# Optimization experiments

Measured on AMD Instinct MI355X. Metric: run time of the kernel, lower is better.

The kernel has to match this reference:

```python
import jax, jax.numpy as jnp
import numpy as np

HIDDEN = 768
META = 25
ED_COUNT = 300
B, N_MENT, N_PAIRS = 2, 2000, 40000


def setup_inputs() -> dict:
    key = jax.random.key(0)
    ks = jax.random.split(key, 8)
    mention_reprs = jax.random.normal(ks[0], (B, N_MENT, HIDDEN), dtype=jnp.float32)
    coref_mention_pairs = jax.random.randint(ks[1], (B, N_PAIRS, 2), 0, N_MENT)
    coref_eds = jax.random.randint(ks[2], (B, N_PAIRS), 0, ED_COUNT)
    in_dim = HIDDEN * 2 + META
    # nn.Linear default init scale ~ 1/sqrt(fan_in); exact init is irrelevant for correctness
    W1 = jax.random.normal(ks[3], (in_dim, HIDDEN), dtype=jnp.float32) / np.sqrt(in_dim)
    b1 = jnp.zeros((HIDDEN,), dtype=jnp.float32)
    W2 = jax.random.normal(ks[4], (HIDDEN, 1), dtype=jnp.float32) / np.sqrt(HIDDEN)
    b2 = jnp.zeros((1,), dtype=jnp.float32)
    ed_table = jax.random.normal(ks[5], (ED_COUNT, META), dtype=jnp.float32)
    return {
        "mention_reprs": mention_reprs,
        "coref_mention_pairs": coref_mention_pairs,
        "coref_eds": coref_eds,
        "ed_table": ed_table,
        "W1": W1,
        "b1": b1,
        "W2": W2,
        "b2": b2,
    }


def reference(mention_reprs, coref_mention_pairs, coref_eds, ed_table, W1, b1, W2, b2):
    b = mention_reprs.shape[0]
    # batch_index gather: [B, P, 2, H]
    bidx = jnp.arange(b)[:, None, None]
    pairs = mention_reprs[bidx, coref_mention_pairs]
    # flatten pair dim -> [B, P, 2H]
    pair_repr = pairs.reshape(b, pairs.shape[1], -1)
    eds = ed_table[coref_eds]  # [B, P, META]
    coref_repr = jnp.concatenate([pair_repr, eds], axis=2)  # [B, P, 2H+META]
    h = jax.nn.relu(coref_repr @ W1 + b1)  # dropout = identity in eval
    logits = (h @ W2 + b2).squeeze(-1)  # [B, P]
    return logits
```

## Files before the change

kernel.cpp:

```cpp
#include <hip/hip_runtime.h>
#include <stdint.h>

#define HIDDEN 768
#define META 25
#define EDC 300
#define BB 2
#define NMENT 2000
#define NPAIRS 40000
#define M_ROWS (BB * NMENT)
#define M_PAD 4096
#define N_OUT 1536
#define TOTAL_PAIRS (BB * NPAIRS)
#define BK 64

typedef __bf16 bf16x8 __attribute__((ext_vector_type(8)));
typedef float f32x4 __attribute__((ext_vector_type(4)));

static __device__ __forceinline__ float bf2f(unsigned short u) {
    union { unsigned int u; float f; } v; v.u = ((unsigned int)u) << 16; return v.f;
}
static __device__ __forceinline__ float2 bf2x(unsigned int u) {
    union { unsigned int x; float f; } lo, hi;
    lo.x = u << 16; hi.x = u & 0xffff0000u;
    float2 r; r.x = lo.f; r.y = hi.f; return r;
}
static __device__ __forceinline__ unsigned short f2bf(float f) {
    union { float f; unsigned int u; } v; v.f = f;
    unsigned int u = v.u;
    unsigned int r = (u + 0x7FFFu + ((u >> 16) & 1u)) >> 16;
    return (unsigned short)r;
}

#define GLOAD_LDS16(g, l)                                                            \
    __builtin_amdgcn_global_load_lds((const __attribute__((address_space(1))) void*)(g), \
                                     (__attribute__((address_space(3))) void*)(l), 16, 0, 0)

#define NB_CONVM 3072
#define NB_CONVW 576
#define NB_PREP  900
#define NB_W2    3

__global__ __launch_bounds__(256) void k_prep_all(
        const float* __restrict__ M, unsigned short* __restrict__ Mb,
        const float* __restrict__ W1, unsigned short* __restrict__ Wt,
        const float* __restrict__ ed_table, const float* __restrict__ b1,
        unsigned short* __restrict__ Epp,
        const float* __restrict__ W2, unsigned short* __restrict__ W2b) {
    const int blk = blockIdx.x;
    const int t = threadIdx.x;
    if (blk < NB_CONVM) {
        int idx = (blk * 256 + t) * 4;
        int row = idx / HIDDEN;
        ushort4 o;
        if (row < M_ROWS) {
            const float4 v = *(const float4*)(M + idx);
            o.x = f2bf(v.x); o.y = f2bf(v.y); o.z = f2bf(v.z); o.w = f2bf(v.w);
        } else {
            o.x = 0; o.y = 0; o.z = 0; o.w = 0;
        }
        *(ushort4*)(Mb + idx) = o;
    } else if (blk < NB_CONVM + NB_CONVW) {
        __shared__ float tile[32][68];
        int id = blk - NB_CONVM;
        int nt = id % 24, kt = id / 24;
        int n0 = nt * 64, k0 = kt * 32;
        int tk = t >> 4, tn = (t & 15) * 4;
        int srcRowOff = (n0 < HIDDEN) ? 0 : HIDDEN;
        int srcColBase = (n0 < HIDDEN) ? n0 : (n0 - HIDDEN);
        {
            const float4 v0 = *(const float4*)(W1 + (size_t)(k0 + tk + srcRowOff) * HIDDEN + srcColBase + tn);
            tile[tk][tn] = v0.x; tile[tk][tn + 1] = v0.y; tile[tk][tn + 2] = v0.z; tile[tk][tn + 3] = v0.w;
            const float4 v1 = *(const float4*)(W1 + (size_t)(k0 + tk + 16 + srcRowOff) * HIDDEN + srcColBase + tn);
            tile[tk + 16][tn] = v1.x; tile[tk + 16][tn + 1] = v1.y; tile[tk + 16][tn + 2] = v1.z; tile[tk + 16][tn + 3] = v1.w;
        }
        __syncthreads();
        int wn = t >> 2, wk = (t & 3) * 8;
        unsigned int p0 = (unsigned int)f2bf(tile[wk + 0][wn]) | ((unsigned int)f2bf(tile[wk + 1][wn]) << 16);
        unsigned int p1 = (unsigned int)f2bf(tile[wk + 2][wn]) | ((unsigned int)f2bf(tile[wk + 3][wn]) << 16);
        unsigned int p2 = (unsigned int)f2bf(tile[wk + 4][wn]) | ((unsigned int)f2bf(tile[wk + 5][wn]) << 16);
        unsigned int p3 = (unsigned int)f2bf(tile[wk + 6][wn]) | ((unsigned int)f2bf(tile[wk + 7][wn]) << 16);
        uint4 pk; pk.x = p0; pk.y = p1; pk.z = p2; pk.w = p3;
        *(uint4*)(Wt + (size_t)(n0 + wn) * HIDDEN + k0 + wk) = pk;
    } else if (blk < NB_CONVM + NB_CONVW + NB_PREP) {
        int id = (blk - NB_CONVM - NB_CONVW) * 256 + t;
        int e = id / HIDDEN, n = id - e * HIDDEN;
        float acc = b1[n];
#pragma unroll
        for (int k = 0; k < META; k++)
            acc += ed_table[e * META + k] * W1[(size_t)(2 * HIDDEN + k) * HIDDEN + n];
        Epp[id] = f2bf(acc);
    } else {
        int id = (blk - NB_CONVM - NB_CONVW - NB_PREP) * 256 + t;
        if (id < HIDDEN) W2b[id] = f2bf(W2[id]);
    }
}

__global__ __launch_bounds__(256) void k_gemm(const unsigned short* __restrict__ Mb,
                                              const unsigned short* __restrict__ Wt,
                                              unsigned short* __restrict__ AW) {
    __shared__ unsigned short As[128 * BK];
    __shared__ unsigned short Bs[64 * BK];
    const int m0 = blockIdx.x * 128;
    const int n0 = blockIdx.y * 64;
    const int t = threadIdx.x, w = t >> 6, lane = t & 63;
    const int wm = (w & 1) * 64, wn = (w >> 1) * 32;
    const int q = lane >> 4, r = lane & 15;
    const int lrow = lane >> 3;
    const int lcol = ((((lane & 7) - lrow) & 7)) * 8;
    const unsigned short* gA = Mb + (size_t)(m0 + w * 32 + lrow) * HIDDEN + lcol;
    const unsigned short* gB = Wt + (size_t)(n0 + w * 16 + lrow) * HIDDEN + lcol;
    unsigned short* lA = As + (w * 32) * BK;
    unsigned short* lB = Bs + (w * 16) * BK;
    f32x4 acc[4][2] = {};
    for (int k0 = 0; k0 < HIDDEN; k0 += BK) {
        GLOAD_LDS16(gA + k0, lA);
        GLOAD_LDS16(gA + k0 + 8 * HIDDEN,  lA + 8 * BK);
        GLOAD_LDS16(gA + k0 + 16 * HIDDEN, lA + 16 * BK);
        GLOAD_LDS16(gA + k0 + 24 * HIDDEN, lA + 24 * BK);
        GLOAD_LDS16(gB + k0, lB);
        GLOAD_LDS16(gB + k0 + 8 * HIDDEN,  lB + 8 * BK);
        __syncthreads();
        bf16x8 af[4][2], bfr[2][2];
        const int rs = r & 7;
#pragma unroll
        for (int i = 0; i < 4; i++)
#pragma unroll
            for (int s = 0; s < 2; s++)
                af[i][s] = *(const bf16x8*)&As[(wm + i * 16 + r) * BK + 8 * ((q + 4 * s + rs) & 7)];
#pragma unroll
        for (int j = 0; j < 2; j++)
#pragma unroll
            for (int s = 0; s < 2; s++)
                bfr[j][s] = *(const bf16x8*)&Bs[(wn + j * 16 + r) * BK + 8 * ((q + 4 * s + rs) & 7)];
#pragma unroll
        for (int i = 0; i < 4; i++)
#pragma unroll
            for (int j = 0; j < 2; j++) {
                acc[i][j] = __builtin_amdgcn_mfma_f32_16x16x32_bf16(af[i][0], bfr[j][0], acc[i][j], 0, 0, 0);
                acc[i][j] = __builtin_amdgcn_mfma_f32_16x16x32_bf16(af[i][1], bfr[j][1], acc[i][j], 0, 0, 0);
            }
        __syncthreads();
    }
    const int colb = n0 + wn + (lane & 15);
    const int rowb = m0 + wm + (lane >> 4) * 4;
#pragma unroll
    for (int i = 0; i < 4; i++)
#pragma unroll
        for (int j = 0; j < 2; j++) {
            unsigned short* dst = AW + (size_t)(rowb + i * 16) * N_OUT + colb + j * 16;
#pragma unroll
            for (int reg = 0; reg < 4; reg++)
                dst[(size_t)reg * N_OUT] = f2bf(acc[i][j][reg]);
        }
}

__global__ __launch_bounds__(256, 6) void k_pair(const unsigned short* __restrict__ AW,
                                                 const unsigned short* __restrict__ Epp,
                                                 const unsigned short* __restrict__ W2b,
                                                 const float* __restrict__ b2,
                                                 const int* __restrict__ pairs,
                                                 const int* __restrict__ eds,
                                                 float* __restrict__ out) {
    const int wid = blockIdx.x * 4 + (threadIdx.x >> 6);
    const int lane = threadIdx.x & 63;
    const int hl = lane & 31;
    const bool lo = lane < 32;
    const int p0 = wid * 2;
    const size_t base = (p0 >= NPAIRS) ? (size_t)NMENT : 0;

    const int4 pr = *(const int4*)(pairs + (size_t)p0 * 2);
    const int2 e2 = *(const int2*)(eds + p0);

    const int n0 = lane * 8;
    const int n1 = 512 + hl * 8;

    const unsigned short* A1a = AW + (base + pr.x) * N_OUT;
    const unsigned short* A2a = AW + (base + pr.y) * N_OUT + HIDDEN;
    const unsigned short* EPa = Epp + (size_t)e2.x * HIDDEN;
    const unsigned short* A1b = AW + (base + pr.z) * N_OUT;
    const unsigned short* A2b = AW + (base + pr.w) * N_OUT + HIDDEN;
    const unsigned short* EPb = Epp + (size_t)e2.y * HIDDEN;

    const unsigned short* t1 = lo ? A1a : A1b;
    const unsigned short* t2 = lo ? A2a : A2b;
    const unsigned short* te = lo ? EPa : EPb;

    uint4 w0 = *(const uint4*)(W2b + n0);
    uint4 wc = *(const uint4*)(W2b + n1);
    uint4 x1 = *(const uint4*)(A1a + n0), x2 = *(const uint4*)(A2a + n0), xe = *(const uint4*)(EPa + n0);
    uint4 y1 = *(const uint4*)(A1b + n0), y2 = *(const uint4*)(A2b + n0), ye = *(const uint4*)(EPb + n0);
    uint4 q1 = *(const uint4*)(t1 + n1),  q2 = *(const uint4*)(t2 + n1),  qe = *(const uint4*)(te + n1);

    float accA = 0.f, accB = 0.f, tacc = 0.f;
#define ACC2(acc, ua, ub, ue, uw)                                              \
    {                                                                          \
        float2 fa = bf2x(ua), fb = bf2x(ub), fe = bf2x(ue), fw = bf2x(uw);     \
        float h0 = fmaxf(fa.x + fb.x + fe.x, 0.f);                             \
        float h1 = fmaxf(fa.y + fb.y + fe.y, 0.f);                             \
        acc += h0 * fw.x + h1 * fw.y;                                          \
    }
    ACC2(accA, x1.x, x2.x, xe.x, w0.x); ACC2(accA, x1.y, x2.y, xe.y, w0.y);
    ACC2(accA, x1.z, x2.z, xe.z, w0.z); ACC2(accA, x1.w, x2.w, xe.w, w0.w);
    ACC2(accB, y1.x, y2.x, ye.x, w0.x); ACC2(accB, y1.y, y2.y, ye.y, w0.y);
    ACC2(accB, y1.z, y2.z, ye.z, w0.z); ACC2(accB, y1.w, y2.w, ye.w, w0.w);
    ACC2(tacc, q1.x, q2.x, qe.x, wc.x); ACC2(tacc, q1.y, q2.y, qe.y, wc.y);
    ACC2(tacc, q1.z, q2.z, qe.z, wc.z); ACC2(tacc, q1.w, q2.w, qe.w, wc.w);
#undef ACC2

#pragma unroll
    for (int o = 32; o > 0; o >>= 1) {
        accA += __shfl_xor(accA, o, 64);
        accB += __shfl_xor(accB, o, 64);
    }
#pragma unroll
    for (int o = 16; o > 0; o >>= 1)
        tacc += __shfl_xor(tacc, o, 64);
    const float tA = __shfl(tacc, 0, 64);
    const float tB = __shfl(tacc, 32, 64);

    if (lane == 0) {
        float bias = b2[0];
        float2 o;
        o.x = accA + tA + bias;
        o.y = accB + tB + bias;
        *(float2*)(out + p0) = o;
    }
}

extern "C" void kernel_launch(void* const* d_in, const int* in_sizes, int n_in,
                              void* d_out, int out_size, void* d_ws, size_t ws_size,
                              hipStream_t stream) {
    const float* mention  = (const float*)d_in[0];
    const int*   pairs    = (const int*)d_in[1];
    const int*   eds      = (const int*)d_in[2];
    const float* ed_table = (const float*)d_in[3];
    const float* W1       = (const float*)d_in[4];
    const float* b1       = (const float*)d_in[5];
    const float* W2       = (const float*)d_in[6];
    const float* b2       = (const float*)d_in[7];
    float* out = (float*)d_out;

    char* ws = (char*)d_ws;
    unsigned short* Mb  = (unsigned short*)(ws);
    unsigned short* Wt  = (unsigned short*)(ws + 6291456);
    unsigned short* AW  = (unsigned short*)(ws + 8650752);
    unsigned short* Epp = (unsigned short*)(ws + 21233664);
    unsigned short* W2b = (unsigned short*)(ws + 21694464);

    k_prep_all<<<dim3(NB_CONVM + NB_CONVW + NB_PREP + NB_W2), dim3(256), 0, stream>>>(
        mention, Mb, W1, Wt, ed_table, b1, Epp, W2, W2b);
    k_gemm<<<dim3(M_PAD / 128, N_OUT / 64), dim3(256), 0, stream>>>(Mb, Wt, AW);
    k_pair<<<dim3(TOTAL_PAIRS / 8), dim3(256), 0, stream>>>(AW, Epp, W2b, b2, pairs, eds, out);
}
```

Baseline: 117.6 us.

## Bucket-sort mention pairs by row locality and swizzle pair blocks across XCDs

Adds a histogram pass (inside the prep kernel) and a scatter kernel that bucket the pairs by coarse first- and second-mention row indices, producing a permutation. The pair kernel walks pairs in that order, so the random row gathers from the projected mention table land on nearby rows. A block-index swizzle hands each XCD a contiguous range of buckets, aiming to raise L2 hit rates on those gathers. The cost is two extra kernel launches, global atomics, and an indirection load per pair, and outputs are now written as scattered scalar stores.

```diff
diff --git a/kernel.cpp b/kernel.cpp
--- a/kernel.cpp
+++ b/kernel.cpp
@@ -12,6 +12,7 @@
 #define N_OUT 1536
 #define TOTAL_PAIRS (BB * NPAIRS)
 #define BK 64
+#define NBUCKET 1024
 
 typedef __bf16 bf16x8 __attribute__((ext_vector_type(8)));
 typedef float f32x4 __attribute__((ext_vector_type(4)));
@@ -31,6 +32,10 @@
     return (unsigned short)r;
 }
 
+static __device__ __forceinline__ int pair_key(int2 pr, int p) {
+    return ((p >= NPAIRS) ? 512 : 0) | ((pr.x >> 6) << 4) | (pr.y >> 7);
+}
+
 #define GLOAD_LDS16(g, l)                                                            \
     __builtin_amdgcn_global_load_lds((const __attribute__((address_space(1))) void*)(g), \
                                      (__attribute__((address_space(3))) void*)(l), 16, 0, 0)
@@ -39,13 +44,20 @@
 #define NB_CONVW 576
 #define NB_PREP  900
 #define NB_W2    3
+#define NB_HIST  40
+
+__global__ __launch_bounds__(256) void k_zero(int* __restrict__ z) {
+#pragma unroll
+    for (int i = 0; i < 8; i++) z[i * 256 + threadIdx.x] = 0;
+}
 
 __global__ __launch_bounds__(256) void k_prep_all(
         const float* __restrict__ M, unsigned short* __restrict__ Mb,
         const float* __restrict__ W1, unsigned short* __restrict__ Wt,
         const float* __restrict__ ed_table, const float* __restrict__ b1,
         unsigned short* __restrict__ Epp,
-        const float* __restrict__ W2, unsigned short* __restrict__ W2b) {
+        const float* __restrict__ W2, unsigned short* __restrict__ W2b,
+        const int* __restrict__ pairs, int* __restrict__ hist) {
     const int blk = blockIdx.x;
     const int t = threadIdx.x;
     if (blk < NB_CONVM) {
@@ -89,9 +101,61 @@
         for (int k = 0; k < META; k++)
             acc += ed_table[e * META + k] * W1[(size_t)(2 * HIDDEN + k) * HIDDEN + n];
         Epp[id] = f2bf(acc);
-    } else {
+    } else if (blk < NB_CONVM + NB_CONVW + NB_PREP + NB_W2) {
         int id = (blk - NB_CONVM - NB_CONVW - NB_PREP) * 256 + t;
         if (id < HIDDEN) W2b[id] = f2bf(W2[id]);
+    } else {
+        __shared__ int lh[NBUCKET];
+        const int hb = blk - (NB_CONVM + NB_CONVW + NB_PREP + NB_W2);
+#pragma unroll
+        for (int i = 0; i < 4; i++) lh[i * 256 + t] = 0;
+        __syncthreads();
+#pragma unroll
+        for (int i = 0; i < 8; i++) {
+            int p = hb * 2048 + i * 256 + t;
+            if (p < TOTAL_PAIRS) {
+                int2 pr = *(const int2*)(pairs + (size_t)p * 2);
+                atomicAdd(&lh[pair_key(pr, p)], 1);
+            }
+        }
+        __syncthreads();
+#pragma unroll
+        for (int i = 0; i < 4; i++) {
+            int v = lh[i * 256 + t];
+            if (v) atomicAdd(&hist[i * 256 + t], v);
+        }
+    }
+}
+
+__global__ __launch_bounds__(256) void k_scatter(const int* __restrict__ pairs,
+                                                 const int* __restrict__ hist,
+                                                 int* __restrict__ cursor,
+                                                 int* __restrict__ perm) {
+    __shared__ int off[NBUCKET];
+    __shared__ int bsum[256];
+    const int t = threadIdx.x;
+    const int4 h = *(const int4*)(hist + t * 4);
+    const int s = h.x + h.y + h.z + h.w;
+    bsum[t] = s;
+    __syncthreads();
+    for (int o = 1; o < 256; o <<= 1) {
+        int v = (t >= o) ? bsum[t - o] : 0;
+        __syncthreads();
+        bsum[t] += v;
+        __syncthreads();
+    }
+    const int excl = bsum[t] - s;
+    off[t * 4 + 0] = excl;
+    off[t * 4 + 1] = excl + h.x;
+    off[t * 4 + 2] = excl + h.x + h.y;
+    off[t * 4 + 3] = excl + h.x + h.y + h.z;
+    __syncthreads();
+    const int p = blockIdx.x * 256 + t;
+    if (p < TOTAL_PAIRS) {
+        const int2 pr = *(const int2*)(pairs + (size_t)p * 2);
+        const int key = pair_key(pr, p);
+        const int rank = atomicAdd(&cursor[key], 1);
+        perm[off[key] + rank] = p;
     }
 }
 
@@ -160,26 +224,33 @@
                                                  const float* __restrict__ b2,
                                                  const int* __restrict__ pairs,
                                                  const int* __restrict__ eds,
+                                                 const int* __restrict__ perm,
                                                  float* __restrict__ out) {
-    const int wid = blockIdx.x * 4 + (threadIdx.x >> 6);
+    const int bi = blockIdx.x;
+    const int wv = threadIdx.x >> 6;
     const int lane = threadIdx.x & 63;
     const int hl = lane & 31;
     const bool lo = lane < 32;
-    const int p0 = wid * 2;
-    const size_t base = (p0 >= NPAIRS) ? (size_t)NMENT : 0;
-
-    const int4 pr = *(const int4*)(pairs + (size_t)p0 * 2);
-    const int2 e2 = *(const int2*)(eds + p0);
+    const int sw = ((bi & 7) * 1250 + (bi >> 3)) * 4 + wv;
+    const int sp0 = sw * 2;
+    const int pa = perm[sp0];
+    const int pb = perm[sp0 + 1];
+    const size_t baseA = (pa >= NPAIRS) ? (size_t)NMENT : 0;
+    const size_t baseB = (pb >= NPAIRS) ? (size_t)NMENT : 0;
+
+    const int2 prA = *(const int2*)(pairs + (size_t)pa * 2);
+    const int2 prB = *(const int2*)(pairs + (size_t)pb * 2);
+    const int edA = eds[pa], edB = eds[pb];
 
     const int n0 = lane * 8;
     const int n1 = 512 + hl * 8;
 
-    const unsigned short* A1a = AW + (base + pr.x) * N_OUT;
-    const unsigned short* A2a = AW + (base + pr.y) * N_OUT + HIDDEN;
-    const unsigned short* EPa = Epp + (size_t)e2.x * HIDDEN;
-    const unsigned short* A1b = AW + (base + pr.z) * N_OUT;
-    const unsigned short* A2b = AW + (base + pr.w) * N_OUT + HIDDEN;
-    const unsigned short* EPb = Epp + (size_t)e2.y * HIDDEN;
+    const unsigned short* A1a = AW + (baseA + prA.x) * N_OUT;
+    const unsigned short* A2a = AW + (baseA + prA.y) * N_OUT + HIDDEN;
+    const unsigned short* EPa = Epp + (size_t)edA * HIDDEN;
+    const unsigned short* A1b = AW + (baseB + prB.x) * N_OUT;
+    const unsigned short* A2b = AW + (baseB + prB.y) * N_OUT + HIDDEN;
+    const unsigned short* EPb = Epp + (size_t)edB * HIDDEN;
 
     const unsigned short* t1 = lo ? A1a : A1b;
     const unsigned short* t2 = lo ? A2a : A2b;
@@ -215,16 +286,9 @@
 #pragma unroll
     for (int o = 16; o > 0; o >>= 1)
         tacc += __shfl_xor(tacc, o, 64);
-    const float tA = __shfl(tacc, 0, 64);
-    const float tB = __shfl(tacc, 32, 64);
-
-    if (lane == 0) {
-        float bias = b2[0];
-        float2 o;
-        o.x = accA + tA + bias;
-        o.y = accB + tB + bias;
-        *(float2*)(out + p0) = o;
-    }
+
+    if (lane == 0)  out[pa] = accA + tacc + b2[0];
+    if (lane == 32) out[pb] = accB + tacc + b2[0];
 }
 
 extern "C" void kernel_launch(void* const* d_in, const int* in_sizes, int n_in,
@@ -246,9 +310,14 @@
     unsigned short* AW  = (unsigned short*)(ws + 8650752);
     unsigned short* Epp = (unsigned short*)(ws + 21233664);
     unsigned short* W2b = (unsigned short*)(ws + 21694464);
-
-    k_prep_all<<<dim3(NB_CONVM + NB_CONVW + NB_PREP + NB_W2), dim3(256), 0, stream>>>(
-        mention, Mb, W1, Wt, ed_table, b1, Epp, W2, W2b);
+    int* hist   = (int*)(ws + 21696000);
+    int* cursor = (int*)(ws + 21700096);
+    int* perm   = (int*)(ws + 21704192);
+
+    k_zero<<<dim3(1), dim3(256), 0, stream>>>(hist);
+    k_prep_all<<<dim3(NB_CONVM + NB_CONVW + NB_PREP + NB_W2 + NB_HIST), dim3(256), 0, stream>>>(
+        mention, Mb, W1, Wt, ed_table, b1, Epp, W2, W2b, pairs, hist);
+    k_scatter<<<dim3((TOTAL_PAIRS + 255) / 256), dim3(256), 0, stream>>>(pairs, hist, cursor, perm);
     k_gemm<<<dim3(M_PAD / 128, N_OUT / 64), dim3(256), 0, stream>>>(Mb, Wt, AW);
-    k_pair<<<dim3(TOTAL_PAIRS / 8), dim3(256), 0, stream>>>(AW, Epp, W2b, b2, pairs, eds, out);
-}
+    k_pair<<<dim3(TOTAL_PAIRS / 8), dim3(256), 0, stream>>>(AW, Epp, W2b, b2, pairs, eds, perm, out);
+}
```

Result: slower. 137.6 us (+17.0%).
